# Kernel tuning notes

Hardware: AMD Instinct MI355X
Metric: run time of the kernel (lower is better)

Reference implementation:

```python
import jax, jax.numpy as jnp
import numpy as np
from jax import lax

N = 262144      # number of coordinate points
CC = 3          # coords_channel
GF = 64         # gating_feature
FEAT = 64       # n_network_features
E = 8           # experts_num
L = 4           # expert_layers
TOPK = 2
BW = 45.0       # bandwidth
LN_EPS = 1e-5
W0S = 0.5 * BW + BW * np.arange(E, dtype=np.float32)  # per-expert first-layer sine freq


def setup_inputs() -> dict:
    key = jax.random.key(0)
    ks = jax.random.split(key, 16)
    u = lambda k, shape, b: jax.random.uniform(k, shape, jnp.float32, -b, b)
    coords = jax.random.normal(ks[0], (N, CC), jnp.float32)
    # first_linear (first_layer_sine_init: U(-1/in, 1/in))
    fw = u(ks[1], (GF, CC), 1.0 / CC)
    fb = u(ks[2], (GF,), 1.0 / CC)
    # gate: Linear(GF,GF) + LayerNorm(GF), Linear(GF,E), softmax
    gw1 = u(ks[3], (GF, GF), np.sqrt(6.0 / GF))
    gb1 = u(ks[4], (GF,), 1.0 / np.sqrt(GF))
    ln_g = jnp.ones((GF,), jnp.float32)
    ln_b = jnp.zeros((GF,), jnp.float32)
    gw2 = u(ks[5], (E, GF), np.sqrt(6.0 / GF))
    gb2 = u(ks[6], (E,), 1.0 / np.sqrt(GF))
    # experts (SIREN): first layer U(-1/in,1/in), rest U(-sqrt(6/in)/30, sqrt(6/in)/30)
    we0 = u(ks[7], (E, FEAT, GF), 1.0 / GF)
    be0 = u(ks[8], (E, FEAT), 1.0 / GF)
    sb = np.sqrt(6.0 / FEAT) / 30.0
    wm = u(ks[9], (L - 2, E, FEAT, FEAT), sb)
    bm = u(ks[10], (L - 2, E, FEAT), sb)
    wl = u(ks[11], (E, FEAT), sb)
    bl = u(ks[12], (E,), sb)
    return {"coords": coords, "fw": fw, "fb": fb, "gw1": gw1, "gb1": gb1,
            "ln_g": ln_g, "ln_b": ln_b, "gw2": gw2, "gb2": gb2,
            "we0": we0, "be0": be0, "wm": wm, "bm": bm, "wl": wl, "bl": bl}


def reference(coords, fw, fb, gw1, gb1, ln_g, ln_b, gw2, gb2, we0, be0, wm, bm, wl, bl):
    w0s = jnp.asarray(W0S)
    # first_linear: [N, GF]
    feature = coords @ fw.T + fb
    # gate: Linear -> LayerNorm -> Linear -> Softmax(dim=1)
    g = feature @ gw1.T + gb1
    mu = jnp.mean(g, axis=-1, keepdims=True)
    var = jnp.mean(jnp.square(g - mu), axis=-1, keepdims=True)
    gn = (g - mu) * lax.rsqrt(var + LN_EPS) * ln_g + ln_b
    index = jax.nn.softmax(gn @ gw2.T + gb2, axis=1)  # [N, E]
    # all experts computed densely on the gated feature: [E, N, FEAT]
    h = jnp.sin(w0s[:, None, None] * (jnp.einsum('nf,ekf->enk', feature, we0) + be0[:, None, :]))
    for l in range(L - 2):
        h = jnp.sin(30.0 * (jnp.einsum('enf,ekf->enk', h, wm[l]) + bm[l][:, None, :]))
    x = (jnp.einsum('enf,ef->en', h, wl) + bl[:, None]).T  # [N, E]
    # top-k mask: ~(index < kth largest) == index >= kth
    kth = lax.top_k(index, TOPK)[0][:, -1:]
    mask = (index >= kth).astype(x.dtype)
    output = jnp.sum(x * mask, axis=1, keepdims=True)  # [N, 1]
    counts = jnp.sum(mask, axis=0)  # per-expert selection counts
    aux_loss = (E / (N * N)) * jnp.dot(counts, counts)
    return output, aux_loss
```

## Files before the change

### kernel.cpp

```cpp
#include <hip/hip_runtime.h>
#include <math.h>

#define NPTS 262144
#define GBLK (NPTS / 128)
#define GGRID (NPTS / 256)
#define CPE  2048
#define TAU  0.01f

typedef float f4v __attribute__((ext_vector_type(4)));
typedef short s8v __attribute__((ext_vector_type(8)));

static __device__ __forceinline__ unsigned short f2bf(float f) {
    unsigned u = __float_as_uint(f);
    u += 0x7fffu + ((u >> 16) & 1u);
    return (unsigned short)(u >> 16);
}
static __device__ __forceinline__ unsigned short f2bf_hw(float f) {
    __bf16 b = (__bf16)f;
    unsigned short u;
    __builtin_memcpy(&u, &b, 2);
    return u;
}
static __device__ __forceinline__ float bf2f(unsigned short h) {
    return __uint_as_float(((unsigned)h) << 16);
}
static __device__ __forceinline__ unsigned pk2b(unsigned short lo, unsigned short hi) {
    return ((unsigned)hi << 16) | (unsigned)lo;
}
static __device__ __forceinline__ unsigned cpack(float lo, float hi) {
    return pk2b(f2bf_hw(lo), f2bf_hw(hi));
}
static __device__ __forceinline__ float sinrev(float x) {
    return __builtin_amdgcn_sinf(x);
}

union BFrag { uint4 q; unsigned u[4]; s8v s; };

__global__ __launch_bounds__(256) void prep_kernel(
    const float* __restrict__ we0, const float* __restrict__ be0,
    const float* __restrict__ wm, const float* __restrict__ bm,
    const float* __restrict__ gw1, const float* __restrict__ gw2,
    uint4* __restrict__ packA, float* __restrict__ biasS,
    uint4* __restrict__ packGW1H, uint4* __restrict__ packGW1L,
    uint4* __restrict__ packGW2H, uint4* __restrict__ packGW2L)
{
    const int idx = blockIdx.x * 256 + threadIdx.x;
    const float PI2I = 0.15915494309189535f;
    if (idx < 12288) {
        const int l = idx & 63;
        const int fr = (idx >> 6) & 7;
        const int grp = idx >> 9;
        const int e = grp / 3, ell = grp % 3;
        const int tau = fr >> 1, ks = fr & 1;
        const int g = l >> 4, m = l & 15;
        const int row = tau * 16 + m;
        const float scale = (ell == 0) ? (22.5f + 45.0f * (float)e) * PI2I : 30.0f * PI2I;
        const float* W = (ell == 0) ? (we0 + e * 4096) : (wm + ((ell - 1) * 8 + e) * 4096);
        unsigned short v[8];
#pragma unroll
        for (int i = 0; i < 8; i++) {
            const int k = 32 * ks + 4 * g + (i < 4 ? i : i + 12);
            v[i] = f2bf(W[row * 64 + k] * scale);
        }
        uint4 q;
        q.x = pk2b(v[0], v[1]); q.y = pk2b(v[2], v[3]);
        q.z = pk2b(v[4], v[5]); q.w = pk2b(v[6], v[7]);
        packA[idx] = q;
    } else if (idx < 13824) {
        const int j = idx - 12288;
        const int r = j & 63;
        const int grp = j >> 6;
        const int e = grp / 3, ell = grp % 3;
        const float scale = (ell == 0) ? (22.5f + 45.0f * (float)e) * PI2I : 30.0f * PI2I;
        const float b = (ell == 0) ? be0[e * 64 + r] : bm[((ell - 1) * 8 + e) * 64 + r];
        biasS[j] = b * scale;
    } else if (idx < 14336) {
        const int j = idx - 13824;
        const int l = j & 63;
        const int fr = j >> 6;
        const int tau = fr >> 1, ks = fr & 1;
        const int g = l >> 4;
        const int row = tau * 16 + (l & 15);
        unsigned short vh[8], vl[8];
#pragma unroll
        for (int i = 0; i < 8; i++) {
            const int k = 32 * ks + 4 * g + (i < 4 ? i : i + 12);
            const float x = gw1[row * 64 + k];
            const unsigned short h = f2bf(x);
            vh[i] = h;
            vl[i] = f2bf(x - bf2f(h));
        }
        uint4 qh, ql;
        qh.x = pk2b(vh[0], vh[1]); qh.y = pk2b(vh[2], vh[3]);
        qh.z = pk2b(vh[4], vh[5]); qh.w = pk2b(vh[6], vh[7]);
        ql.x = pk2b(vl[0], vl[1]); ql.y = pk2b(vl[2], vl[3]);
        ql.z = pk2b(vl[4], vl[5]); ql.w = pk2b(vl[6], vl[7]);
        packGW1H[j] = qh; packGW1L[j] = ql;
    } else if (idx < 14464) {
        const int j = idx - 14336;
        const int l = j & 63;
        const int ks = j >> 6;
        const int g = l >> 4;
        const int row = l & 15;
        unsigned short vh[8], vl[8];
#pragma unroll
        for (int i = 0; i < 8; i++) {
            const int k = 32 * ks + 4 * g + (i < 4 ? i : i + 12);
            const float x = (row < 8) ? gw2[row * 64 + k] : 0.f;
            const unsigned short h = f2bf(x);
            vh[i] = h;
            vl[i] = f2bf(x - bf2f(h));
        }
        uint4 qh, ql;
        qh.x = pk2b(vh[0], vh[1]); qh.y = pk2b(vh[2], vh[3]);
        qh.z = pk2b(vh[4], vh[5]); qh.w = pk2b(vh[6], vh[7]);
        ql.x = pk2b(vl[0], vl[1]); ql.y = pk2b(vl[2], vl[3]);
        ql.z = pk2b(vl[4], vl[5]); ql.w = pk2b(vl[6], vl[7]);
        packGW2H[j] = qh; packGW2L[j] = ql;
    }
}

__global__ __launch_bounds__(512, 2) void gate_kernel(
    const float* __restrict__ coords,
    const float* __restrict__ fw, const float* __restrict__ fb,
    const float* __restrict__ gb1, const float* __restrict__ lng,
    const float* __restrict__ lnb, const float* __restrict__ gb2,
    const uint4* __restrict__ packGW1H, const uint4* __restrict__ packGW1L,
    const uint4* __restrict__ packGW2H, const uint4* __restrict__ packGW2L,
    unsigned char* __restrict__ sel, int* __restrict__ blkcnt,
    int* __restrict__ reflist, int* __restrict__ refcnt)
{
    __shared__ float s_fw[192], s_fb[64], s_gb1[64], s_lng[64], s_lnb[64], s_gb2[8];
    __shared__ uint4 sW1H[512], sW1L[512];
    __shared__ uint4 sW2H[128], sW2L[128];
    __shared__ int s_cnt[2][8];
    const int t = threadIdx.x;
    sW1H[t] = packGW1H[t];
    sW1L[t] = packGW1L[t];
    if (t < 128) { sW2H[t] = packGW2H[t]; sW2L[t] = packGW2L[t]; }
    if (t < 192) s_fw[t] = fw[t];
    if (t < 64) { s_fb[t] = fb[t]; s_gb1[t] = gb1[t]; s_lng[t] = lng[t]; s_lnb[t] = lnb[t]; }
    if (t < 8) s_gb2[t] = gb2[t];
    if (t < 16) s_cnt[t >> 3][t & 7] = 0;
    __syncthreads();

    const int lane = t & 63;
    const int wv = t >> 6;
    const int g = lane >> 4, c = lane & 15;
    const int half = wv >> 2;
    const int n0 = blockIdx.x * 256 + wv * 32 + c;
    const int n1 = n0 + 16;

    const float a0 = coords[n0 * 3], a1 = coords[n0 * 3 + 1], a2 = coords[n0 * 3 + 2];
    const float b0 = coords[n1 * 3], b1 = coords[n1 * 3 + 1], b2 = coords[n1 * 3 + 2];
    BFrag Bh0[2], Bl0[2], Bh1[2], Bl1[2];
#pragma unroll
    for (int ks = 0; ks < 2; ks++) {
#pragma unroll
        for (int q = 0; q < 4; q++) {
            const int i0 = ks * 8 + 2 * q, i1 = i0 + 1;
            const int s0 = i0 >> 2, j0 = i0 & 3;
            const int s1 = i1 >> 2, j1 = i1 & 3;
            const int k0 = 16 * s0 + 4 * g + j0;
            const int k1 = 16 * s1 + 4 * g + j1;
            const float w0x = s_fw[k0 * 3], w0y = s_fw[k0 * 3 + 1], w0z = s_fw[k0 * 3 + 2];
            const float w1x = s_fw[k1 * 3], w1y = s_fw[k1 * 3 + 1], w1z = s_fw[k1 * 3 + 2];
            const float bb0 = s_fb[k0], bb1 = s_fb[k1];
            const float p0 = bb0 + a0 * w0x + a1 * w0y + a2 * w0z;
            const float p1 = bb1 + a0 * w1x + a1 * w1y + a2 * w1z;
            const float q0 = bb0 + b0 * w0x + b1 * w0y + b2 * w0z;
            const float q1 = bb1 + b0 * w1x + b1 * w1y + b2 * w1z;
            const unsigned short ph0 = f2bf_hw(p0), ph1 = f2bf_hw(p1);
            const unsigned short qh0 = f2bf_hw(q0), qh1 = f2bf_hw(q1);
            Bh0[ks].u[q] = pk2b(ph0, ph1);
            Bl0[ks].u[q] = cpack(p0 - bf2f(ph0), p1 - bf2f(ph1));
            Bh1[ks].u[q] = pk2b(qh0, qh1);
            Bl1[ks].u[q] = cpack(q0 - bf2f(qh0), q1 - bf2f(qh1));
        }
    }

    f4v acc0[4], acc1[4];
#pragma unroll
    for (int tau = 0; tau < 4; tau++) {
        const float4 b = *(const float4*)&s_gb1[tau * 16 + 4 * g];
        acc0[tau][0] = b.x; acc0[tau][1] = b.y; acc0[tau][2] = b.z; acc0[tau][3] = b.w;
        acc1[tau][0] = b.x; acc1[tau][1] = b.y; acc1[tau][2] = b.z; acc1[tau][3] = b.w;
    }
#pragma unroll
    for (int tau = 0; tau < 4; tau++) {
        BFrag AH0, AH1, AL0, AL1;
        AH0.q = sW1H[(tau * 2 + 0) * 64 + lane];
        AH1.q = sW1H[(tau * 2 + 1) * 64 + lane];
        AL0.q = sW1L[(tau * 2 + 0) * 64 + lane];
        AL1.q = sW1L[(tau * 2 + 1) * 64 + lane];
        acc0[tau] = __builtin_amdgcn_mfma_f32_16x16x32_bf16(AH0.s, Bh0[0].s, acc0[tau], 0, 0, 0);
        acc1[tau] = __builtin_amdgcn_mfma_f32_16x16x32_bf16(AH0.s, Bh1[0].s, acc1[tau], 0, 0, 0);
        acc0[tau] = __builtin_amdgcn_mfma_f32_16x16x32_bf16(AH1.s, Bh0[1].s, acc0[tau], 0, 0, 0);
        acc1[tau] = __builtin_amdgcn_mfma_f32_16x16x32_bf16(AH1.s, Bh1[1].s, acc1[tau], 0, 0, 0);
        acc0[tau] = __builtin_amdgcn_mfma_f32_16x16x32_bf16(AH0.s, Bl0[0].s, acc0[tau], 0, 0, 0);
        acc1[tau] = __builtin_amdgcn_mfma_f32_16x16x32_bf16(AH0.s, Bl1[0].s, acc1[tau], 0, 0, 0);
        acc0[tau] = __builtin_amdgcn_mfma_f32_16x16x32_bf16(AH1.s, Bl0[1].s, acc0[tau], 0, 0, 0);
        acc1[tau] = __builtin_amdgcn_mfma_f32_16x16x32_bf16(AH1.s, Bl1[1].s, acc1[tau], 0, 0, 0);
        acc0[tau] = __builtin_amdgcn_mfma_f32_16x16x32_bf16(AL0.s, Bh0[0].s, acc0[tau], 0, 0, 0);
        acc1[tau] = __builtin_amdgcn_mfma_f32_16x16x32_bf16(AL0.s, Bh1[0].s, acc1[tau], 0, 0, 0);
        acc0[tau] = __builtin_amdgcn_mfma_f32_16x16x32_bf16(AL1.s, Bh0[1].s, acc0[tau], 0, 0, 0);
        acc1[tau] = __builtin_amdgcn_mfma_f32_16x16x32_bf16(AL1.s, Bh1[1].s, acc1[tau], 0, 0, 0);
    }

    float s1a = 0.f, s1b = 0.f;
#pragma unroll
    for (int tau = 0; tau < 4; tau++)
#pragma unroll
        for (int j = 0; j < 4; j++) { s1a += acc0[tau][j]; s1b += acc1[tau][j]; }
    s1a += __shfl_xor(s1a, 16, 64); s1a += __shfl_xor(s1a, 32, 64);
    s1b += __shfl_xor(s1b, 16, 64); s1b += __shfl_xor(s1b, 32, 64);
    const float mu0 = s1a * (1.f / 64.f), mu1 = s1b * (1.f / 64.f);
    float s2a = 0.f, s2b = 0.f;
#pragma unroll
    for (int tau = 0; tau < 4; tau++)
#pragma unroll
        for (int j = 0; j < 4; j++) {
            const float d0 = acc0[tau][j] - mu0; s2a += d0 * d0;
            const float d1 = acc1[tau][j] - mu1; s2b += d1 * d1;
        }
    s2a += __shfl_xor(s2a, 16, 64); s2a += __shfl_xor(s2a, 32, 64);
    s2b += __shfl_xor(s2b, 16, 64); s2b += __shfl_xor(s2b, 32, 64);
    const float rs0 = rsqrtf(s2a * (1.f / 64.f) + 1e-5f);
    const float rs1 = rsqrtf(s2b * (1.f / 64.f) + 1e-5f);

    BFrag Gh0[2], Gl0[2], Gh1[2], Gl1[2];
#pragma unroll
    for (int ks = 0; ks < 2; ks++) {
#pragma unroll
        for (int q = 0; q < 4; q++) {
            const int i0 = ks * 8 + 2 * q, i1 = i0 + 1;
            const int tau0 = i0 >> 2, j0 = i0 & 3;
            const int tau1 = i1 >> 2, j1 = i1 & 3;
            const int r0 = tau0 * 16 + 4 * g + j0;
            const int r1 = tau1 * 16 + 4 * g + j1;
            const float gnA0 = (acc0[tau0][j0] - mu0) * rs0 * s_lng[r0] + s_lnb[r0];
            const float gnA1 = (acc0[tau1][j1] - mu0) * rs0 * s_lng[r1] + s_lnb[r1];
            const float gnB0 = (acc1[tau0][j0] - mu1) * rs1 * s_lng[r0] + s_lnb[r0];
            const float gnB1 = (acc1[tau1][j1] - mu1) * rs1 * s_lng[r1] + s_lnb[r1];
            const unsigned short hA0 = f2bf_hw(gnA0), hA1 = f2bf_hw(gnA1);
            const unsigned short hB0 = f2bf_hw(gnB0), hB1 = f2bf_hw(gnB1);
            Gh0[ks].u[q] = pk2b(hA0, hA1);
            Gl0[ks].u[q] = cpack(gnA0 - bf2f(hA0), gnA1 - bf2f(hA1));
            Gh1[ks].u[q] = pk2b(hB0, hB1);
            Gl1[ks].u[q] = cpack(gnB0 - bf2f(hB0), gnB1 - bf2f(hB1));
        }
    }

    f4v lacc0 = {0.f, 0.f, 0.f, 0.f}, lacc1 = {0.f, 0.f, 0.f, 0.f};
    {
        BFrag W0, W1, V0, V1;
        W0.q = sW2H[0 * 64 + lane]; W1.q = sW2H[1 * 64 + lane];
        V0.q = sW2L[0 * 64 + lane]; V1.q = sW2L[1 * 64 + lane];
        lacc0 = __builtin_amdgcn_mfma_f32_16x16x32_bf16(W0.s, Gh0[0].s, lacc0, 0, 0, 0);
        lacc1 = __builtin_amdgcn_mfma_f32_16x16x32_bf16(W0.s, Gh1[0].s, lacc1, 0, 0, 0);
        lacc0 = __builtin_amdgcn_mfma_f32_16x16x32_bf16(W1.s, Gh0[1].s, lacc0, 0, 0, 0);
        lacc1 = __builtin_amdgcn_mfma_f32_16x16x32_bf16(W1.s, Gh1[1].s, lacc1, 0, 0, 0);
        lacc0 = __builtin_amdgcn_mfma_f32_16x16x32_bf16(W0.s, Gl0[0].s, lacc0, 0, 0, 0);
        lacc1 = __builtin_amdgcn_mfma_f32_16x16x32_bf16(W0.s, Gl1[0].s, lacc1, 0, 0, 0);
        lacc0 = __builtin_amdgcn_mfma_f32_16x16x32_bf16(W1.s, Gl0[1].s, lacc0, 0, 0, 0);
        lacc1 = __builtin_amdgcn_mfma_f32_16x16x32_bf16(W1.s, Gl1[1].s, lacc1, 0, 0, 0);
        lacc0 = __builtin_amdgcn_mfma_f32_16x16x32_bf16(V0.s, Gh0[0].s, lacc0, 0, 0, 0);
        lacc1 = __builtin_amdgcn_mfma_f32_16x16x32_bf16(V0.s, Gh1[0].s, lacc1, 0, 0, 0);
        lacc0 = __builtin_amdgcn_mfma_f32_16x16x32_bf16(V1.s, Gh0[1].s, lacc0, 0, 0, 0);
        lacc1 = __builtin_amdgcn_mfma_f32_16x16x32_bf16(V1.s, Gh1[1].s, lacc1, 0, 0, 0);
    }

    float logit0[8], logit1[8];
#pragma unroll
    for (int j = 0; j < 4; j++) {
        const float o0 = __shfl_xor(lacc0[j], 16, 64);
        const float o1 = __shfl_xor(lacc1[j], 16, 64);
        logit0[j] = lacc0[j] + s_gb2[j];
        logit0[4 + j] = o0 + s_gb2[4 + j];
        logit1[j] = lacc1[j] + s_gb2[j];
        logit1[4 + j] = o1 + s_gb2[4 + j];
    }

    unsigned mbits0 = 0, mbits1 = 0;
    bool flg0, flg1;
    {
        float m1 = logit0[0]; int i1 = 0;
#pragma unroll
        for (int e = 1; e < 8; e++) if (logit0[e] > m1) { m1 = logit0[e]; i1 = e; }
        float m2 = -INFINITY; int i2 = -1;
#pragma unroll
        for (int e = 0; e < 8; e++) if (e != i1 && logit0[e] > m2) { m2 = logit0[e]; i2 = e; }
        float m3 = -INFINITY;
#pragma unroll
        for (int e = 0; e < 8; e++) if (e != i1 && e != i2 && logit0[e] > m3) m3 = logit0[e];
#pragma unroll
        for (int e = 0; e < 8; e++) if (logit0[e] >= m2) mbits0 |= 1u << e;
        flg0 = (m2 - m3 < TAU);
    }
    {
        float m1 = logit1[0]; int i1 = 0;
#pragma unroll
        for (int e = 1; e < 8; e++) if (logit1[e] > m1) { m1 = logit1[e]; i1 = e; }
        float m2 = -INFINITY; int i2 = -1;
#pragma unroll
        for (int e = 0; e < 8; e++) if (e != i1 && logit1[e] > m2) { m2 = logit1[e]; i2 = e; }
        float m3 = -INFINITY;
#pragma unroll
        for (int e = 0; e < 8; e++) if (e != i1 && e != i2 && logit1[e] > m3) m3 = logit1[e];
#pragma unroll
        for (int e = 0; e < 8; e++) if (logit1[e] >= m2) mbits1 |= 1u << e;
        flg1 = (m2 - m3 < TAU);
    }

    const bool active = (g == 0);
    if (active) { sel[n0] = (unsigned char)mbits0; sel[n1] = (unsigned char)mbits1; }

#pragma unroll
    for (int e = 0; e < 8; e++) {
        const unsigned long long bal0 = __ballot(active && ((mbits0 >> e) & 1u));
        const unsigned long long bal1 = __ballot(active && ((mbits1 >> e) & 1u));
        if (lane == 0) atomicAdd(&s_cnt[half][e], (int)(__popcll(bal0) + __popcll(bal1)));
    }
    {
        const unsigned long long bal0 = __ballot(active && flg0);
        const unsigned long long bal1 = __ballot(active && flg1);
        const int p0 = (int)__popcll(bal0);
        int pos0 = 0;
        if (lane == 0 && (bal0 | bal1)) pos0 = atomicAdd(refcnt, p0 + (int)__popcll(bal1));
        pos0 = __shfl(pos0, 0, 64);
        if (active && flg0) {
            const int rank = (int)__popcll(bal0 & ((1ull << lane) - 1ull));
            reflist[pos0 + rank] = n0;
        }
        if (active && flg1) {
            const int rank = p0 + (int)__popcll(bal1 & ((1ull << lane) - 1ull));
            reflist[pos0 + rank] = n1;
        }
    }
    __syncthreads();
    if (t < 16) blkcnt[blockIdx.x * 16 + t] = s_cnt[t >> 3][t & 7];
}

__global__ __launch_bounds__(256) void refine_kernel(
    const float* __restrict__ coords,
    const float* __restrict__ fw, const float* __restrict__ fb,
    const float* __restrict__ gw1, const float* __restrict__ gb1,
    const float* __restrict__ lng, const float* __restrict__ lnb,
    const float* __restrict__ gw2, const float* __restrict__ gb2,
    const int* __restrict__ reflist, const int* __restrict__ refcnt,
    unsigned char* __restrict__ sel, int* __restrict__ blkcnt)
{
    const int R = *refcnt;
    if (blockIdx.x * 4 >= R) return;

    __shared__ float s_gw1t[64 * 65];
    __shared__ float s_gw2[512];
    __shared__ float s_fw[192], s_fb[64], s_gb1[64], s_lng[64], s_lnb[64], s_gb2[8];
    __shared__ float s_f[4][64];

    const int t = threadIdx.x;
    for (int i = t; i < 4096; i += 256) s_gw1t[(i & 63) * 65 + (i >> 6)] = gw1[i];
    for (int i = t; i < 512; i += 256) s_gw2[i] = gw2[i];
    if (t < 192) s_fw[t] = fw[t];
    if (t < 64) { s_fb[t] = fb[t]; s_gb1[t] = gb1[t]; s_lng[t] = lng[t]; s_lnb[t] = lnb[t]; }
    if (t < 8) s_gb2[t] = gb2[t];
    __syncthreads();

    const int wv = t >> 6, lane = t & 63;
    for (int idx = blockIdx.x * 4 + wv; idx < R; idx += gridDim.x * 4) {
        const int n = reflist[idx];
        const float c0 = coords[n * 3], c1 = coords[n * 3 + 1], c2 = coords[n * 3 + 2];
        const float fr = s_fb[lane] + c0 * s_fw[lane * 3] + c1 * s_fw[lane * 3 + 1]
                       + c2 * s_fw[lane * 3 + 2];
        s_f[wv][lane] = fr;
        float a = s_gb1[lane];
#pragma unroll
        for (int k = 0; k < 64; k++)
            a += s_f[wv][k] * s_gw1t[k * 65 + lane];
        float mu = a;
#pragma unroll
        for (int d = 1; d < 64; d <<= 1) mu += __shfl_xor(mu, d, 64);
        mu *= (1.f / 64.f);
        const float dv = a - mu;
        float v = dv * dv;
#pragma unroll
        for (int d = 1; d < 64; d <<= 1) v += __shfl_xor(v, d, 64);
        const float rs = rsqrtf(v * (1.f / 64.f) + 1e-5f);
        const float gn = dv * rs * s_lng[lane] + s_lnb[lane];
        float lp[8];
#pragma unroll
        for (int e = 0; e < 8; e++) lp[e] = gn * s_gw2[e * 64 + lane];
#pragma unroll
        for (int e = 0; e < 8; e++) {
#pragma unroll
            for (int d = 1; d < 64; d <<= 1) lp[e] += __shfl_xor(lp[e], d, 64);
            lp[e] += s_gb2[e];
        }
        if (lane == 0) {
            float m1 = lp[0]; int i1 = 0;
#pragma unroll
            for (int e = 1; e < 8; e++) if (lp[e] > m1) { m1 = lp[e]; i1 = e; }
            float m2 = -INFINITY;
#pragma unroll
            for (int e = 0; e < 8; e++) if (e != i1 && lp[e] > m2) m2 = lp[e];
            unsigned mbits = 0;
#pragma unroll
            for (int e = 0; e < 8; e++) if (lp[e] >= m2) mbits |= 1u << e;
            const unsigned old = sel[n];
            if (mbits != old) {
                sel[n] = (unsigned char)mbits;
                const int b = n >> 7;
#pragma unroll
                for (int e = 0; e < 8; e++) {
                    const int was = (old >> e) & 1, now = (mbits >> e) & 1;
                    if (was != now) atomicAdd(&blkcnt[b * 8 + e], now - was);
                }
            }
        }
    }
}

__global__ __launch_bounds__(256) void scan_kernel(
    const int* __restrict__ blkcnt, int* __restrict__ baseoff,
    int* __restrict__ counts)
{
    const int e = blockIdx.x;
    const int t = threadIdx.x;
    const int lane = t & 63, wv = t >> 6;
    __shared__ int s_w[4];

    int v[8]; int sum = 0;
#pragma unroll
    for (int i = 0; i < 8; i++) { v[i] = blkcnt[(t * 8 + i) * 8 + e]; sum += v[i]; }
    int incl = sum;
#pragma unroll
    for (int d = 1; d < 64; d <<= 1) {
        const int x = __shfl_up(incl, d, 64);
        if (lane >= d) incl += x;
    }
    if (lane == 63) s_w[wv] = incl;
    __syncthreads();
    int woff = 0;
#pragma unroll
    for (int i = 0; i < 4; i++) if (i < wv) woff += s_w[i];
    int run = woff + incl - sum;
#pragma unroll
    for (int i = 0; i < 8; i++) { baseoff[(t * 8 + i) * 8 + e] = run; run += v[i]; }
    if (t == 255) counts[e] = run;
}

__global__ __launch_bounds__(128) void scatter_kernel(
    const unsigned char* __restrict__ sel, const int* __restrict__ baseoff,
    const int* __restrict__ counts, int* __restrict__ buckets, float* __restrict__ out)
{
    __shared__ int s_w0[8];
    const int t = threadIdx.x;
    const int n = blockIdx.x * 128 + t;
    out[n] = 0.f;
    if (blockIdx.x == 0 && t == 0) {
        double s = 0.0;
        for (int e = 0; e < 8; e++) { const double c = (double)counts[e]; s += c * c; }
        out[NPTS] = (float)(8.0 * s / ((double)NPTS * (double)NPTS));
    }
    const unsigned m = sel[n];
    const int w = t >> 6, lane = t & 63;
    unsigned long long bal[8];
#pragma unroll
    for (int e = 0; e < 8; e++) {
        bal[e] = __ballot((m >> e) & 1u);
        if (w == 0 && lane == 0) s_w0[e] = (int)__popcll(bal[e]);
    }
    __syncthreads();
#pragma unroll
    for (int e = 0; e < 8; e++) {
        if ((m >> e) & 1u) {
            int rank = (int)__popcll(bal[e] & ((1ull << lane) - 1ull));
            if (w == 1) rank += s_w0[e];
            buckets[e * NPTS + baseoff[blockIdx.x * 8 + e] + rank] = n;
        }
    }
}

__global__ __launch_bounds__(256) void expert_kernel(
    const float* __restrict__ coords,
    const float* __restrict__ fw, const float* __restrict__ fb,
    const float* __restrict__ wl, const float* __restrict__ bl,
    const uint4* __restrict__ packA, const float* __restrict__ biasS,
    const int* __restrict__ counts, const int* __restrict__ buckets,
    float* __restrict__ out)
{
    const int e = blockIdx.x >> 11;
    const int chunk = blockIdx.x & (CPE - 1);
    const int cnt = counts[e];
    const int base = chunk * 128;
    if (base >= cnt) return;

    __shared__ float s_b[192];
    __shared__ float s_wl[64];
    __shared__ float s_fw[192];
    __shared__ float s_fb[64];
    __shared__ float s_bl;

    const int t = threadIdx.x;
    if (t < 192) {
        s_b[t] = biasS[e * 192 + t];
        s_fw[t] = fw[t];
    }
    if (t < 64) {
        s_fb[t] = fb[t];
        s_wl[t] = wl[e * 64 + t];
    }
    if (t == 0) s_bl = bl[e];
    __syncthreads();

    const int lane = t & 63;
    const int wv = t >> 6;
    const int g = lane >> 4, c = lane & 15;
    const int i0 = base + wv * 32 + c;
    const int i1 = i0 + 16;
    const int id0 = (i0 < cnt) ? buckets[e * NPTS + i0] : -1;
    const int id1 = (i1 < cnt) ? buckets[e * NPTS + i1] : -1;

    BFrag B0[2], B1[2];
    {
        const float a0 = (id0 >= 0) ? coords[id0 * 3] : 0.f;
        const float a1 = (id0 >= 0) ? coords[id0 * 3 + 1] : 0.f;
        const float a2 = (id0 >= 0) ? coords[id0 * 3 + 2] : 0.f;
        const float b0 = (id1 >= 0) ? coords[id1 * 3] : 0.f;
        const float b1 = (id1 >= 0) ? coords[id1 * 3 + 1] : 0.f;
        const float b2 = (id1 >= 0) ? coords[id1 * 3 + 2] : 0.f;
        float f0[4][4], f1[4][4];
#pragma unroll
        for (int s = 0; s < 4; s++) {
#pragma unroll
            for (int j = 0; j < 4; j++) {
                const int k = 16 * s + 4 * g + j;
                const float wx = s_fw[k * 3], wy = s_fw[k * 3 + 1], wz = s_fw[k * 3 + 2];
                const float bb = s_fb[k];
                f0[s][j] = bb + a0 * wx + a1 * wy + a2 * wz;
                f1[s][j] = bb + b0 * wx + b1 * wy + b2 * wz;
            }
        }
#pragma unroll
        for (int ks = 0; ks < 2; ks++) {
            B0[ks].u[0] = cpack(f0[2 * ks][0], f0[2 * ks][1]);
            B0[ks].u[1] = cpack(f0[2 * ks][2], f0[2 * ks][3]);
            B0[ks].u[2] = cpack(f0[2 * ks + 1][0], f0[2 * ks + 1][1]);
            B0[ks].u[3] = cpack(f0[2 * ks + 1][2], f0[2 * ks + 1][3]);
            B1[ks].u[0] = cpack(f1[2 * ks][0], f1[2 * ks][1]);
            B1[ks].u[1] = cpack(f1[2 * ks][2], f1[2 * ks][3]);
            B1[ks].u[2] = cpack(f1[2 * ks + 1][0], f1[2 * ks + 1][1]);
            B1[ks].u[3] = cpack(f1[2 * ks + 1][2], f1[2 * ks + 1][3]);
        }
    }

#pragma unroll 1
    for (int ell = 0; ell < 2; ell++) {
        f4v acc0[4], acc1[4];
#pragma unroll
        for (int tau = 0; tau < 4; tau++) {
            const float4 b = *(const float4*)&s_b[ell * 64 + tau * 16 + 4 * g];
            acc0[tau][0] = b.x; acc0[tau][1] = b.y; acc0[tau][2] = b.z; acc0[tau][3] = b.w;
            acc1[tau][0] = b.x; acc1[tau][1] = b.y; acc1[tau][2] = b.z; acc1[tau][3] = b.w;
        }
        const uint4* Ab = packA + (size_t)((e * 3 + ell) * 8) * 64 + lane;
#pragma unroll
        for (int tau = 0; tau < 4; tau++) {
            BFrag A0, A1;
            A0.q = Ab[(tau * 2 + 0) * 64];
            A1.q = Ab[(tau * 2 + 1) * 64];
            acc0[tau] = __builtin_amdgcn_mfma_f32_16x16x32_bf16(A0.s, B0[0].s, acc0[tau], 0, 0, 0);
            acc0[tau] = __builtin_amdgcn_mfma_f32_16x16x32_bf16(A1.s, B0[1].s, acc0[tau], 0, 0, 0);
            acc1[tau] = __builtin_amdgcn_mfma_f32_16x16x32_bf16(A0.s, B1[0].s, acc1[tau], 0, 0, 0);
            acc1[tau] = __builtin_amdgcn_mfma_f32_16x16x32_bf16(A1.s, B1[1].s, acc1[tau], 0, 0, 0);
        }
#pragma unroll
        for (int ks = 0; ks < 2; ks++) {
            B0[ks].u[0] = cpack(sinrev(acc0[2 * ks][0]), sinrev(acc0[2 * ks][1]));
            B0[ks].u[1] = cpack(sinrev(acc0[2 * ks][2]), sinrev(acc0[2 * ks][3]));
            B0[ks].u[2] = cpack(sinrev(acc0[2 * ks + 1][0]), sinrev(acc0[2 * ks + 1][1]));
            B0[ks].u[3] = cpack(sinrev(acc0[2 * ks + 1][2]), sinrev(acc0[2 * ks + 1][3]));
            B1[ks].u[0] = cpack(sinrev(acc1[2 * ks][0]), sinrev(acc1[2 * ks][1]));
            B1[ks].u[1] = cpack(sinrev(acc1[2 * ks][2]), sinrev(acc1[2 * ks][3]));
            B1[ks].u[2] = cpack(sinrev(acc1[2 * ks + 1][0]), sinrev(acc1[2 * ks + 1][1]));
            B1[ks].u[3] = cpack(sinrev(acc1[2 * ks + 1][2]), sinrev(acc1[2 * ks + 1][3]));
        }
    }

    {
        f4v acc0[4], acc1[4];
#pragma unroll
        for (int tau = 0; tau < 4; tau++) {
            const float4 b = *(const float4*)&s_b[2 * 64 + tau * 16 + 4 * g];
            acc0[tau][0] = b.x; acc0[tau][1] = b.y; acc0[tau][2] = b.z; acc0[tau][3] = b.w;
            acc1[tau][0] = b.x; acc1[tau][1] = b.y; acc1[tau][2] = b.z; acc1[tau][3] = b.w;
        }
        const uint4* Ab = packA + (size_t)((e * 3 + 2) * 8) * 64 + lane;
#pragma unroll
        for (int tau = 0; tau < 4; tau++) {
            BFrag A0, A1;
            A0.q = Ab[(tau * 2 + 0) * 64];
            A1.q = Ab[(tau * 2 + 1) * 64];
            acc0[tau] = __builtin_amdgcn_mfma_f32_16x16x32_bf16(A0.s, B0[0].s, acc0[tau], 0, 0, 0);
            acc0[tau] = __builtin_amdgcn_mfma_f32_16x16x32_bf16(A1.s, B0[1].s, acc0[tau], 0, 0, 0);
            acc1[tau] = __builtin_amdgcn_mfma_f32_16x16x32_bf16(A0.s, B1[0].s, acc1[tau], 0, 0, 0);
            acc1[tau] = __builtin_amdgcn_mfma_f32_16x16x32_bf16(A1.s, B1[1].s, acc1[tau], 0, 0, 0);
        }
        float px0 = 0.f, px1 = 0.f;
#pragma unroll
        for (int tau = 0; tau < 4; tau++) {
            const float4 w = *(const float4*)&s_wl[tau * 16 + 4 * g];
            px0 += sinrev(acc0[tau][0]) * w.x + sinrev(acc0[tau][1]) * w.y
                 + sinrev(acc0[tau][2]) * w.z + sinrev(acc0[tau][3]) * w.w;
            px1 += sinrev(acc1[tau][0]) * w.x + sinrev(acc1[tau][1]) * w.y
                 + sinrev(acc1[tau][2]) * w.z + sinrev(acc1[tau][3]) * w.w;
        }
        px0 += __shfl_xor(px0, 16, 64); px0 += __shfl_xor(px0, 32, 64);
        px1 += __shfl_xor(px1, 16, 64); px1 += __shfl_xor(px1, 32, 64);
        if (g == 0) {
            if (id0 >= 0) atomicAdd(&out[id0], px0 + s_bl);
            if (id1 >= 0) atomicAdd(&out[id1], px1 + s_bl);
        }
    }
}

extern "C" void kernel_launch(void* const* d_in, const int* in_sizes, int n_in,
                              void* d_out, int out_size, void* d_ws, size_t ws_size,
                              hipStream_t stream)
{
    const float* coords = (const float*)d_in[0];
    const float* fw  = (const float*)d_in[1];
    const float* fb  = (const float*)d_in[2];
    const float* gw1 = (const float*)d_in[3];
    const float* gb1 = (const float*)d_in[4];
    const float* lng = (const float*)d_in[5];
    const float* lnb = (const float*)d_in[6];
    const float* gw2 = (const float*)d_in[7];
    const float* gb2 = (const float*)d_in[8];
    const float* we0 = (const float*)d_in[9];
    const float* be0 = (const float*)d_in[10];
    const float* wm  = (const float*)d_in[11];
    const float* bm  = (const float*)d_in[12];
    const float* wl  = (const float*)d_in[13];
    const float* bl  = (const float*)d_in[14];
    float* out = (float*)d_out;

    char* ws = (char*)d_ws;
    int* counts           = (int*)ws;
    int* buckets          = (int*)(ws + 64);
    uint4* packA          = (uint4*)(ws + 8388672);
    float* biasS          = (float*)(ws + 8585280);
    int* blkcnt           = (int*)(ws + 8591424);
    int* baseoff          = (int*)(ws + 8656960);
    unsigned char* sel    = (unsigned char*)(ws + 8722496);
    uint4* packGW1H       = (uint4*)(ws + 8984640);
    uint4* packGW1L       = (uint4*)(ws + 8992832);
    uint4* packGW2H       = (uint4*)(ws + 9001024);
    uint4* packGW2L       = (uint4*)(ws + 9003072);
    int* reflist          = (int*)(ws + 9005120);
    int* refcnt           = (int*)(ws + 10053696);

    hipMemsetAsync(refcnt, 0, 64, stream);

    prep_kernel<<<57, 256, 0, stream>>>(we0, be0, wm, bm, gw1, gw2, packA, biasS,
                                        packGW1H, packGW1L, packGW2H, packGW2L);
    gate_kernel<<<GGRID, 512, 0, stream>>>(coords, fw, fb, gb1, lng, lnb, gb2,
                                           packGW1H, packGW1L, packGW2H, packGW2L,
                                           sel, blkcnt, reflist, refcnt);
    refine_kernel<<<128, 256, 0, stream>>>(coords, fw, fb, gw1, gb1, lng, lnb, gw2, gb2,
                                           reflist, refcnt, sel, blkcnt);
    scan_kernel<<<8, 256, 0, stream>>>(blkcnt, baseoff, counts);
    scatter_kernel<<<GBLK, 128, 0, stream>>>(sel, baseoff, counts, buckets, out);
    expert_kernel<<<8 * CPE, 256, 0, stream>>>(coords, fw, fb, wl, bl, packA, biasS,
                                               counts, buckets, out);
}
```

Before: 104.3 us.

## Fold gate first linear into first_linear via precomputed 64x3 matrix

Because feature is an affine map of the 3-D coordinates, the gate's first Linear (64x64) is composed with first_linear on the device in double precision into a 64x3 matrix plus bias. The gate kernel then computes the pre-LayerNorm activations with a few scalar FMAs per row, replacing the split-bf16 MFMA GEMM and its packed weights. The refcnt reset moves from a memset into the prep kernel, and the gate launch changes from 512- to 256-thread blocks over twice as many blocks, with refine getting more blocks. Composing the two linears changes rounding slightly, which may flip which points fall near top-k ties and need refinement.

```diff
diff --git a/kernel.cpp b/kernel.cpp
--- a/kernel.cpp
+++ b/kernel.cpp
@@ -3,7 +3,6 @@
 
 #define NPTS 262144
 #define GBLK (NPTS / 128)
-#define GGRID (NPTS / 256)
 #define CPE  2048
 #define TAU  0.01f
 
@@ -40,9 +39,11 @@
     const float* __restrict__ we0, const float* __restrict__ be0,
     const float* __restrict__ wm, const float* __restrict__ bm,
     const float* __restrict__ gw1, const float* __restrict__ gw2,
+    const float* __restrict__ fw, const float* __restrict__ fb,
+    const float* __restrict__ gb1,
     uint4* __restrict__ packA, float* __restrict__ biasS,
-    uint4* __restrict__ packGW1H, uint4* __restrict__ packGW1L,
-    uint4* __restrict__ packGW2H, uint4* __restrict__ packGW2L)
+    uint4* __restrict__ packGW2H, uint4* __restrict__ packGW2L,
+    float* __restrict__ M1, float* __restrict__ b1p, int* __restrict__ refcnt)
 {
     const int idx = blockIdx.x * 256 + threadIdx.x;
     const float PI2I = 0.15915494309189535f;
@@ -74,30 +75,8 @@
         const float scale = (ell == 0) ? (22.5f + 45.0f * (float)e) * PI2I : 30.0f * PI2I;
         const float b = (ell == 0) ? be0[e * 64 + r] : bm[((ell - 1) * 8 + e) * 64 + r];
         biasS[j] = b * scale;
-    } else if (idx < 14336) {
+    } else if (idx < 13952) {
         const int j = idx - 13824;
-        const int l = j & 63;
-        const int fr = j >> 6;
-        const int tau = fr >> 1, ks = fr & 1;
-        const int g = l >> 4;
-        const int row = tau * 16 + (l & 15);
-        unsigned short vh[8], vl[8];
-#pragma unroll
-        for (int i = 0; i < 8; i++) {
-            const int k = 32 * ks + 4 * g + (i < 4 ? i : i + 12);
-            const float x = gw1[row * 64 + k];
-            const unsigned short h = f2bf(x);
-            vh[i] = h;
-            vl[i] = f2bf(x - bf2f(h));
-        }
-        uint4 qh, ql;
-        qh.x = pk2b(vh[0], vh[1]); qh.y = pk2b(vh[2], vh[3]);
-        qh.z = pk2b(vh[4], vh[5]); qh.w = pk2b(vh[6], vh[7]);
-        ql.x = pk2b(vl[0], vl[1]); ql.y = pk2b(vl[2], vl[3]);
-        ql.z = pk2b(vl[4], vl[5]); ql.w = pk2b(vl[6], vl[7]);
-        packGW1H[j] = qh; packGW1L[j] = ql;
-    } else if (idx < 14464) {
-        const int j = idx - 14336;
         const int l = j & 63;
         const int ks = j >> 6;
         const int g = l >> 4;
@@ -117,112 +96,72 @@
         ql.x = pk2b(vl[0], vl[1]); ql.y = pk2b(vl[2], vl[3]);
         ql.z = pk2b(vl[4], vl[5]); ql.w = pk2b(vl[6], vl[7]);
         packGW2H[j] = qh; packGW2L[j] = ql;
-    }
-}
-
-__global__ __launch_bounds__(512, 2) void gate_kernel(
+    } else if (idx < 14144) {
+        const int m = idx - 13952;
+        const int r = m / 3, d = m % 3;
+        double s = 0.0;
+        for (int j = 0; j < 64; j++) s += (double)gw1[r * 64 + j] * (double)fw[j * 3 + d];
+        M1[m] = (float)s;
+    } else if (idx < 14208) {
+        const int r = idx - 14144;
+        double s = (double)gb1[r];
+        for (int j = 0; j < 64; j++) s += (double)gw1[r * 64 + j] * (double)fb[j];
+        b1p[r] = (float)s;
+    } else if (idx == 14208) {
+        *refcnt = 0;
+    }
+}
+
+__global__ __launch_bounds__(256) void gate_kernel(
     const float* __restrict__ coords,
-    const float* __restrict__ fw, const float* __restrict__ fb,
-    const float* __restrict__ gb1, const float* __restrict__ lng,
-    const float* __restrict__ lnb, const float* __restrict__ gb2,
-    const uint4* __restrict__ packGW1H, const uint4* __restrict__ packGW1L,
+    const float* __restrict__ M1, const float* __restrict__ b1p,
+    const float* __restrict__ lng, const float* __restrict__ lnb,
+    const float* __restrict__ gb2,
     const uint4* __restrict__ packGW2H, const uint4* __restrict__ packGW2L,
     unsigned char* __restrict__ sel, int* __restrict__ blkcnt,
     int* __restrict__ reflist, int* __restrict__ refcnt)
 {
-    __shared__ float s_fw[192], s_fb[64], s_gb1[64], s_lng[64], s_lnb[64], s_gb2[8];
-    __shared__ uint4 sW1H[512], sW1L[512];
+    __shared__ float s_M1[192], s_b1p[64], s_lng[64], s_lnb[64], s_gb2[8];
     __shared__ uint4 sW2H[128], sW2L[128];
-    __shared__ int s_cnt[2][8];
+    __shared__ int s_cnt[8];
     const int t = threadIdx.x;
-    sW1H[t] = packGW1H[t];
-    sW1L[t] = packGW1L[t];
     if (t < 128) { sW2H[t] = packGW2H[t]; sW2L[t] = packGW2L[t]; }
-    if (t < 192) s_fw[t] = fw[t];
-    if (t < 64) { s_fb[t] = fb[t]; s_gb1[t] = gb1[t]; s_lng[t] = lng[t]; s_lnb[t] = lnb[t]; }
-    if (t < 8) s_gb2[t] = gb2[t];
-    if (t < 16) s_cnt[t >> 3][t & 7] = 0;
+    if (t < 192) s_M1[t] = M1[t];
+    if (t < 64) { s_b1p[t] = b1p[t]; s_lng[t] = lng[t]; s_lnb[t] = lnb[t]; }
+    if (t < 8) { s_gb2[t] = gb2[t]; s_cnt[t] = 0; }
     __syncthreads();
 
     const int lane = t & 63;
     const int wv = t >> 6;
     const int g = lane >> 4, c = lane & 15;
-    const int half = wv >> 2;
-    const int n0 = blockIdx.x * 256 + wv * 32 + c;
+    const int n0 = blockIdx.x * 128 + wv * 32 + c;
     const int n1 = n0 + 16;
 
     const float a0 = coords[n0 * 3], a1 = coords[n0 * 3 + 1], a2 = coords[n0 * 3 + 2];
     const float b0 = coords[n1 * 3], b1 = coords[n1 * 3 + 1], b2 = coords[n1 * 3 + 2];
-    BFrag Bh0[2], Bl0[2], Bh1[2], Bl1[2];
-#pragma unroll
-    for (int ks = 0; ks < 2; ks++) {
-#pragma unroll
-        for (int q = 0; q < 4; q++) {
-            const int i0 = ks * 8 + 2 * q, i1 = i0 + 1;
-            const int s0 = i0 >> 2, j0 = i0 & 3;
-            const int s1 = i1 >> 2, j1 = i1 & 3;
-            const int k0 = 16 * s0 + 4 * g + j0;
-            const int k1 = 16 * s1 + 4 * g + j1;
-            const float w0x = s_fw[k0 * 3], w0y = s_fw[k0 * 3 + 1], w0z = s_fw[k0 * 3 + 2];
-            const float w1x = s_fw[k1 * 3], w1y = s_fw[k1 * 3 + 1], w1z = s_fw[k1 * 3 + 2];
-            const float bb0 = s_fb[k0], bb1 = s_fb[k1];
-            const float p0 = bb0 + a0 * w0x + a1 * w0y + a2 * w0z;
-            const float p1 = bb1 + a0 * w1x + a1 * w1y + a2 * w1z;
-            const float q0 = bb0 + b0 * w0x + b1 * w0y + b2 * w0z;
-            const float q1 = bb1 + b0 * w1x + b1 * w1y + b2 * w1z;
-            const unsigned short ph0 = f2bf_hw(p0), ph1 = f2bf_hw(p1);
-            const unsigned short qh0 = f2bf_hw(q0), qh1 = f2bf_hw(q1);
-            Bh0[ks].u[q] = pk2b(ph0, ph1);
-            Bl0[ks].u[q] = cpack(p0 - bf2f(ph0), p1 - bf2f(ph1));
-            Bh1[ks].u[q] = pk2b(qh0, qh1);
-            Bl1[ks].u[q] = cpack(q0 - bf2f(qh0), q1 - bf2f(qh1));
-        }
-    }
-
-    f4v acc0[4], acc1[4];
-#pragma unroll
-    for (int tau = 0; tau < 4; tau++) {
-        const float4 b = *(const float4*)&s_gb1[tau * 16 + 4 * g];
-        acc0[tau][0] = b.x; acc0[tau][1] = b.y; acc0[tau][2] = b.z; acc0[tau][3] = b.w;
-        acc1[tau][0] = b.x; acc1[tau][1] = b.y; acc1[tau][2] = b.z; acc1[tau][3] = b.w;
-    }
-#pragma unroll
-    for (int tau = 0; tau < 4; tau++) {
-        BFrag AH0, AH1, AL0, AL1;
-        AH0.q = sW1H[(tau * 2 + 0) * 64 + lane];
-        AH1.q = sW1H[(tau * 2 + 1) * 64 + lane];
-        AL0.q = sW1L[(tau * 2 + 0) * 64 + lane];
-        AL1.q = sW1L[(tau * 2 + 1) * 64 + lane];
-        acc0[tau] = __builtin_amdgcn_mfma_f32_16x16x32_bf16(AH0.s, Bh0[0].s, acc0[tau], 0, 0, 0);
-        acc1[tau] = __builtin_amdgcn_mfma_f32_16x16x32_bf16(AH0.s, Bh1[0].s, acc1[tau], 0, 0, 0);
-        acc0[tau] = __builtin_amdgcn_mfma_f32_16x16x32_bf16(AH1.s, Bh0[1].s, acc0[tau], 0, 0, 0);
-        acc1[tau] = __builtin_amdgcn_mfma_f32_16x16x32_bf16(AH1.s, Bh1[1].s, acc1[tau], 0, 0, 0);
-        acc0[tau] = __builtin_amdgcn_mfma_f32_16x16x32_bf16(AH0.s, Bl0[0].s, acc0[tau], 0, 0, 0);
-        acc1[tau] = __builtin_amdgcn_mfma_f32_16x16x32_bf16(AH0.s, Bl1[0].s, acc1[tau], 0, 0, 0);
-        acc0[tau] = __builtin_amdgcn_mfma_f32_16x16x32_bf16(AH1.s, Bl0[1].s, acc0[tau], 0, 0, 0);
-        acc1[tau] = __builtin_amdgcn_mfma_f32_16x16x32_bf16(AH1.s, Bl1[1].s, acc1[tau], 0, 0, 0);
-        acc0[tau] = __builtin_amdgcn_mfma_f32_16x16x32_bf16(AL0.s, Bh0[0].s, acc0[tau], 0, 0, 0);
-        acc1[tau] = __builtin_amdgcn_mfma_f32_16x16x32_bf16(AL0.s, Bh1[0].s, acc1[tau], 0, 0, 0);
-        acc0[tau] = __builtin_amdgcn_mfma_f32_16x16x32_bf16(AL1.s, Bh0[1].s, acc0[tau], 0, 0, 0);
-        acc1[tau] = __builtin_amdgcn_mfma_f32_16x16x32_bf16(AL1.s, Bh1[1].s, acc1[tau], 0, 0, 0);
+
+    float ga[16], gb[16];
+#pragma unroll
+    for (int i = 0; i < 16; i++) {
+        const int r = ((i >> 2) << 4) + 4 * g + (i & 3);
+        const float m0 = s_M1[r * 3], m1 = s_M1[r * 3 + 1], m2 = s_M1[r * 3 + 2];
+        const float bb = s_b1p[r];
+        ga[i] = bb + a0 * m0 + a1 * m1 + a2 * m2;
+        gb[i] = bb + b0 * m0 + b1 * m1 + b2 * m2;
     }
 
     float s1a = 0.f, s1b = 0.f;
 #pragma unroll
-    for (int tau = 0; tau < 4; tau++)
-#pragma unroll
-        for (int j = 0; j < 4; j++) { s1a += acc0[tau][j]; s1b += acc1[tau][j]; }
+    for (int i = 0; i < 16; i++) { s1a += ga[i]; s1b += gb[i]; }
     s1a += __shfl_xor(s1a, 16, 64); s1a += __shfl_xor(s1a, 32, 64);
     s1b += __shfl_xor(s1b, 16, 64); s1b += __shfl_xor(s1b, 32, 64);
     const float mu0 = s1a * (1.f / 64.f), mu1 = s1b * (1.f / 64.f);
     float s2a = 0.f, s2b = 0.f;
 #pragma unroll
-    for (int tau = 0; tau < 4; tau++)
-#pragma unroll
-        for (int j = 0; j < 4; j++) {
-            const float d0 = acc0[tau][j] - mu0; s2a += d0 * d0;
-            const float d1 = acc1[tau][j] - mu1; s2b += d1 * d1;
-        }
+    for (int i = 0; i < 16; i++) {
+        const float d0 = ga[i] - mu0; s2a += d0 * d0;
+        const float d1 = gb[i] - mu1; s2b += d1 * d1;
+    }
     s2a += __shfl_xor(s2a, 16, 64); s2a += __shfl_xor(s2a, 32, 64);
     s2b += __shfl_xor(s2b, 16, 64); s2b += __shfl_xor(s2b, 32, 64);
     const float rs0 = rsqrtf(s2a * (1.f / 64.f) + 1e-5f);
@@ -234,14 +173,12 @@
 #pragma unroll
         for (int q = 0; q < 4; q++) {
             const int i0 = ks * 8 + 2 * q, i1 = i0 + 1;
-            const int tau0 = i0 >> 2, j0 = i0 & 3;
-            const int tau1 = i1 >> 2, j1 = i1 & 3;
-            const int r0 = tau0 * 16 + 4 * g + j0;
-            const int r1 = tau1 * 16 + 4 * g + j1;
-            const float gnA0 = (acc0[tau0][j0] - mu0) * rs0 * s_lng[r0] + s_lnb[r0];
-            const float gnA1 = (acc0[tau1][j1] - mu0) * rs0 * s_lng[r1] + s_lnb[r1];
-            const float gnB0 = (acc1[tau0][j0] - mu1) * rs1 * s_lng[r0] + s_lnb[r0];
-            const float gnB1 = (acc1[tau1][j1] - mu1) * rs1 * s_lng[r1] + s_lnb[r1];
+            const int r0 = ((i0 >> 2) << 4) + 4 * g + (i0 & 3);
+            const int r1 = ((i1 >> 2) << 4) + 4 * g + (i1 & 3);
+            const float gnA0 = (ga[i0] - mu0) * rs0 * s_lng[r0] + s_lnb[r0];
+            const float gnA1 = (ga[i1] - mu0) * rs0 * s_lng[r1] + s_lnb[r1];
+            const float gnB0 = (gb[i0] - mu1) * rs1 * s_lng[r0] + s_lnb[r0];
+            const float gnB1 = (gb[i1] - mu1) * rs1 * s_lng[r1] + s_lnb[r1];
             const unsigned short hA0 = f2bf_hw(gnA0), hA1 = f2bf_hw(gnA1);
             const unsigned short hB0 = f2bf_hw(gnB0), hB1 = f2bf_hw(gnB1);
             Gh0[ks].u[q] = pk2b(hA0, hA1);
@@ -319,7 +256,7 @@
     for (int e = 0; e < 8; e++) {
         const unsigned long long bal0 = __ballot(active && ((mbits0 >> e) & 1u));
         const unsigned long long bal1 = __ballot(active && ((mbits1 >> e) & 1u));
-        if (lane == 0) atomicAdd(&s_cnt[half][e], (int)(__popcll(bal0) + __popcll(bal1)));
+        if (lane == 0) atomicAdd(&s_cnt[e], (int)(__popcll(bal0) + __popcll(bal1)));
     }
     {
         const unsigned long long bal0 = __ballot(active && flg0);
@@ -338,7 +275,7 @@
         }
     }
     __syncthreads();
-    if (t < 16) blkcnt[blockIdx.x * 16 + t] = s_cnt[t >> 3][t & 7];
+    if (t < 8) blkcnt[blockIdx.x * 8 + t] = s_cnt[t];
 }
 
 __global__ __launch_bounds__(256) void refine_kernel(
@@ -653,21 +590,19 @@
     int* blkcnt           = (int*)(ws + 8591424);
     int* baseoff          = (int*)(ws + 8656960);
     unsigned char* sel    = (unsigned char*)(ws + 8722496);
-    uint4* packGW1H       = (uint4*)(ws + 8984640);
-    uint4* packGW1L       = (uint4*)(ws + 8992832);
-    uint4* packGW2H       = (uint4*)(ws + 9001024);
-    uint4* packGW2L       = (uint4*)(ws + 9003072);
-    int* reflist          = (int*)(ws + 9005120);
-    int* refcnt           = (int*)(ws + 10053696);
-
-    hipMemsetAsync(refcnt, 0, 64, stream);
-
-    prep_kernel<<<57, 256, 0, stream>>>(we0, be0, wm, bm, gw1, gw2, packA, biasS,
-                                        packGW1H, packGW1L, packGW2H, packGW2L);
-    gate_kernel<<<GGRID, 512, 0, stream>>>(coords, fw, fb, gb1, lng, lnb, gb2,
-                                           packGW1H, packGW1L, packGW2H, packGW2L,
-                                           sel, blkcnt, reflist, refcnt);
-    refine_kernel<<<128, 256, 0, stream>>>(coords, fw, fb, gw1, gb1, lng, lnb, gw2, gb2,
+    uint4* packGW2H       = (uint4*)(ws + 8984640);
+    uint4* packGW2L       = (uint4*)(ws + 8986688);
+    int* reflist          = (int*)(ws + 8988736);
+    int* refcnt           = (int*)(ws + 10037312);
+    float* M1             = (float*)(ws + 10037376);
+    float* b1p            = (float*)(ws + 10038144);
+
+    prep_kernel<<<58, 256, 0, stream>>>(we0, be0, wm, bm, gw1, gw2, fw, fb, gb1,
+                                        packA, biasS, packGW2H, packGW2L, M1, b1p, refcnt);
+    gate_kernel<<<GBLK, 256, 0, stream>>>(coords, M1, b1p, lng, lnb, gb2,
+                                          packGW2H, packGW2L,
+                                          sel, blkcnt, reflist, refcnt);
+    refine_kernel<<<256, 256, 0, stream>>>(coords, fw, fb, gw1, gb1, lng, lnb, gw2, gb2,
                                            reflist, refcnt, sel, blkcnt);
     scan_kernel<<<8, 256, 0, stream>>>(blkcnt, baseoff, counts);
     scatter_kernel<<<GBLK, 128, 0, stream>>>(sel, baseoff, counts, buckets, out);
```

Result: faster. 93.35 us (-10.5%).
